# Kernel tuning notes

Hardware: AMD Instinct MI355X
Metric: run time of the kernel (lower is better)

Reference implementation:

```python
import jax, jax.numpy as jnp
import numpy as np

N_NODES = 100000
N_EDGES = 1600000


def _sage_conv(x, src, dst, W_l, W_r, b):
    """PyG SAGEConv (mean aggr): lin_l(mean of neighbor feats) + b + lin_r(x)."""
    n = x.shape[0]
    msgs = x[src]                                            # [E, F] gather
    agg = jax.ops.segment_sum(msgs, dst, num_segments=n)     # [N, F]
    cnt = jax.ops.segment_sum(jnp.ones((src.shape[0],), x.dtype), dst,
                              num_segments=n)                # [N]
    mean = agg / jnp.maximum(cnt, 1.0)[:, None]
    return mean @ W_l + b + x @ W_r


def setup_inputs() -> dict:
    key = jax.random.key(0)
    ks = jax.random.split(key, 8)
    x = jax.random.normal(ks[0], (N_NODES, 64), dtype=jnp.float32)
    edge_index = jax.random.randint(ks[1], (2, N_EDGES), 0, N_NODES, dtype=jnp.int64)
    # Glorot-ish small init for weights
    W1_l = jax.random.normal(ks[2], (64, 128), dtype=jnp.float32) * 0.1
    W1_r = jax.random.normal(ks[3], (64, 128), dtype=jnp.float32) * 0.1
    b1 = jax.random.normal(ks[4], (128,), dtype=jnp.float32) * 0.1
    W2_l = jax.random.normal(ks[5], (128, 64), dtype=jnp.float32) * 0.1
    W2_r = jax.random.normal(ks[6], (128, 64), dtype=jnp.float32) * 0.1
    b2 = jax.random.normal(ks[7], (64,), dtype=jnp.float32) * 0.1
    return {"x": x, "edge_index": edge_index, "W1_l": W1_l, "W1_r": W1_r,
            "b1": b1, "W2_l": W2_l, "W2_r": W2_r, "b2": b2}


def reference(x, edge_index, W1_l, W1_r, b1, W2_l, W2_r, b2):
    src, dst = edge_index[0], edge_index[1]
    h = jax.nn.relu(_sage_conv(x, src, dst, W1_l, W1_r, b1))  # [N, 128]
    out = _sage_conv(h, src, dst, W2_l, W2_r, b2)             # [N, 64]
    return out
```

## Files before the change

kernel.cpp:

```cpp
#include <hip/hip_runtime.h>
#include <hip/hip_bf16.h>
#include <stdint.h>


typedef unsigned short u16;
typedef __attribute__((ext_vector_type(8))) short short8;
typedef __attribute__((ext_vector_type(4))) float f32x4;

#define BSHIFT 9
#define BSIZE  512
#define CHUNK  8192
#define NCP    256

__device__ __forceinline__ float bf2f(u16 v) { return __uint_as_float(((uint32_t)v) << 16); }
__device__ __forceinline__ float bfu_lo(uint32_t u) { return __uint_as_float(u << 16); }
__device__ __forceinline__ float bfu_hi(uint32_t u) { return __uint_as_float(u & 0xffff0000u); }
__device__ __forceinline__ u16 f2bf(float f) {
    uint32_t u = __float_as_uint(f);
    return (u16)((u + 0x7fffu + ((u >> 16) & 1u)) >> 16);
}

__global__ __launch_bounds__(512) void setup_k(
    const void* __restrict__ x, const void* __restrict__ ei,
    const void* __restrict__ W1l, const void* __restrict__ W1r,
    const void* __restrict__ b1, const void* __restrict__ W2l,
    const void* __restrict__ W2r, const void* __restrict__ b2,
    u16* __restrict__ wpk, u16* __restrict__ xb,
    int* __restrict__ hist2d, int* __restrict__ flags,
    int nn, int ne, int nb, int nchunk, int ncvt,
    int c0, int c1, int c2, int c3, int c4, int c5, int c6) {
    __shared__ int sh[512];
    __shared__ int sflag;
    int bid = blockIdx.x, tid = threadIdx.x;
    if (bid < nchunk) {
        sh[tid] = 0;
        int samp = 0;
        if (tid < 32) {
            long long n32 = 2LL * ne;
            long long stride = n32 / 32; if (stride < 1) stride = 1;
            long long i = (long long)tid * stride; i |= 1;
            if (i >= n32) i = 1;
            samp = (((const int*)ei)[i] != 0);
        }
        unsigned long long m = __ballot(samp);
        if (tid == 0) sflag = (m == 0ULL) ? 1 : 0;
        __syncthreads();
        int e64 = sflag;
        int base = bid * CHUNK;
#pragma unroll
        for (int j = 0; j < 16; j++) {
            int e = base + j * 512 + tid;
            if (e < ne) {
                int dst = e64 ? (int)((const long long*)ei)[(size_t)ne + e]
                              : ((const int*)ei)[(size_t)ne + e];
                if ((unsigned)dst < (unsigned)nn) atomicAdd(&sh[dst >> BSHIFT], 1);
            }
        }
        __syncthreads();
        for (int b = tid; b < nb; b += 512)
            hist2d[b * NCP + bid] = sh[b];
    } else if (bid < nchunk + ncvt) {
        int samp = 0;
        if (tid < 32) {
            int C = c0; int stride = C / 32; if (stride < 1) stride = 1;
            long long i = (long long)tid * stride;
            if (i > C - 1) i = C - 1; i &= ~1LL;
            u16 v = ((const u16*)x)[i];
            int e = (v >> 7) & 0xFF;
            samp = ((e >= 0x50 && e <= 0x97) || v == 0) ? 1 : 0;
        }
        unsigned long long m = __ballot(samp);
        if (tid == 0) sflag = (__popcll(m) >= 24) ? 1 : 0;
        __syncthreads();
        if (sflag) return;
        int i = (bid - nchunk) * 512 + tid;
        if (i < nn * 16) {
            float4 f = ((const float4*)x)[i];
            *(ushort4*)&xb[(size_t)i * 4] =
                make_ushort4(f2bf(f.x), f2bf(f.y), f2bf(f.z), f2bf(f.w));
        }
    } else if (bid < nchunk + ncvt + 4) {
        int b = bid - nchunk - ncvt;
        const void* src = (b == 0) ? W1l : (b == 1) ? W1r : (b == 2) ? W2l : W2r;
        int C = (b == 0) ? c1 : (b == 1) ? c2 : (b == 2) ? c4 : c5;
        int samp = 0;
        if (tid < 32) {
            int stride = C / 32; if (stride < 1) stride = 1;
            long long i = (long long)tid * stride;
            if (i > C - 1) i = C - 1; i &= ~1LL;
            u16 v = ((const u16*)src)[i];
            int e = (v >> 7) & 0xFF;
            samp = ((e >= 0x50 && e <= 0x97) || v == 0) ? 1 : 0;
        }
        unsigned long long m = __ballot(samp);
        if (tid == 0) sflag = (__popcll(m) >= 24) ? 1 : 0;
        __syncthreads();
        int isbf = sflag;
        u16* dst = wpk + ((b >= 2) ? (16384 + (b - 2) * 8192) : 0);
        for (int i = tid; i < 2048; i += 512) {
            u16 v0, v1, v2, v3;
            if (isbf) {
                ushort4 u = ((const ushort4*)src)[i];
                v0 = u.x; v1 = u.y; v2 = u.z; v3 = u.w;
            } else {
                float4 u = ((const float4*)src)[i];
                v0 = f2bf(u.x); v1 = f2bf(u.y); v2 = f2bf(u.z); v3 = f2bf(u.w);
            }
            int k, n, k8;
            if (b <= 1) { k = i >> 5; n = (i & 31) * 4; k8 = (b == 1 ? 8 : 0) + (k >> 3); }
            else        { k = i >> 4; n = (i & 15) * 4; k8 = k >> 3; }
            int kc = k8 >> 2, q = k8 & 3, w = k & 7;
            int basei = ((n >> 4) * 4 + kc) * 512 + (q * 16 + (n & 15)) * 8 + w;
            dst[basei] = v0; dst[basei + 8] = v1; dst[basei + 16] = v2; dst[basei + 24] = v3;
        }
    } else {
        int a = tid >> 5, lane = tid & 31;
        if (tid < 8) sh[tid] = 0;
        __syncthreads();
        if (a < 7) {
            const void* ptrs[7] = {x, W1l, W1r, b1, W2l, W2r, b2};
            int cs[7] = {c0, c1, c2, c3, c4, c5, c6};
            int C = cs[a];
            int stride = C / 32; if (stride < 1) stride = 1;
            long long i = (long long)lane * stride;
            if (i > C - 1) i = C - 1;
            i &= ~1LL;
            u16 v = ((const u16*)ptrs[a])[i];
            int e = (v >> 7) & 0xFF;
            int sane = ((e >= 0x50 && e <= 0x97) || v == 0) ? 1 : 0;
            atomicAdd(&sh[a], sane);
        } else if (a == 7) {
            long long n32 = 2LL * ne;
            long long stride = n32 / 32; if (stride < 1) stride = 1;
            long long i = (long long)lane * stride; i |= 1;
            if (i >= n32) i = 1;
            int wv = ((const int*)ei)[i];
            atomicAdd(&sh[7], wv != 0 ? 1 : 0);
        }
        __syncthreads();
        if (tid < 7) flags[tid] = (sh[tid] >= 24) ? 1 : 0;
        if (tid == 7) flags[7] = (sh[7] == 0) ? 1 : 0;
    }
}

__global__ __launch_bounds__(256) void scan2d(
    const int* __restrict__ hist2d, int* __restrict__ base2d,
    int* __restrict__ btot, int nchunk) {
    __shared__ int t0[256];
    int b = blockIdx.x, tid = threadIdx.x;
    int v = (tid < nchunk) ? hist2d[b * NCP + tid] : 0;
    t0[tid] = v;
    __syncthreads();
    for (int d = 1; d < 256; d <<= 1) {
        int t = (tid >= d) ? t0[tid - d] : 0;
        __syncthreads();
        t0[tid] += t;
        __syncthreads();
    }
    if (tid < nchunk) base2d[b * NCP + tid] = t0[tid] - v;
    if (tid == 255) btot[b] = t0[255];
}

__global__ __launch_bounds__(512) void partition_k(
    const void* __restrict__ ei, const int* __restrict__ btot,
    const int* __restrict__ base2d,
    unsigned* __restrict__ ep, int nn, int ne, int nb) {
    __shared__ unsigned stage[CHUNK];
    __shared__ u16 ab[CHUNK];
    __shared__ int hist[512], incl[512], exl[512], gbase[512], lcur[512];
    __shared__ int e64s;
    int tid = threadIdx.x;
    int base = blockIdx.x * CHUNK;
    hist[tid] = 0;
    int samp = 0;
    if (tid < 32) {
        long long n32 = 2LL * ne;
        long long stride = n32 / 32; if (stride < 1) stride = 1;
        long long i = (long long)tid * stride; i |= 1;
        if (i >= n32) i = 1;
        samp = (((const int*)ei)[i] != 0);
    }
    unsigned long long bm = __ballot(samp);
    if (tid == 0) e64s = (bm == 0ULL) ? 1 : 0;
    __syncthreads();
    int e64 = e64s;
    unsigned pk[16]; int bk[16];
#pragma unroll
    for (int j = 0; j < 16; j++) {
        int e = base + j * 512 + tid;
        bk[j] = -1;
        pk[j] = 0;
        if (e < ne) {
            int src, dst;
            if (e64) {
                src = (int)((const long long*)ei)[e];
                dst = (int)((const long long*)ei)[(size_t)ne + e];
            } else {
                src = ((const int*)ei)[e];
                dst = ((const int*)ei)[(size_t)ne + e];
            }
            if ((unsigned)dst < (unsigned)nn) {
                if ((unsigned)src >= (unsigned)nn) src = 0;
                bk[j] = dst >> BSHIFT;
                pk[j] = (unsigned)src | ((unsigned)(dst & (BSIZE - 1)) << 17);
                atomicAdd(&hist[bk[j]], 1);
            }
        }
    }
    __syncthreads();
    incl[tid] = hist[tid];
    __syncthreads();
    for (int d = 1; d < 512; d <<= 1) {
        int t = (tid >= d) ? incl[tid - d] : 0;
        __syncthreads();
        incl[tid] += t;
        __syncthreads();
    }
    int ex = incl[tid] - hist[tid];
    exl[tid] = ex;
    lcur[tid] = ex;
    int tot = incl[511];
    __syncthreads();
    incl[tid] = (tid < nb) ? btot[tid] : 0;
    __syncthreads();
    for (int d = 1; d < 512; d <<= 1) {
        int t = (tid >= d) ? incl[tid - d] : 0;
        __syncthreads();
        incl[tid] += t;
        __syncthreads();
    }
    int bo_t = incl[tid] - ((tid < nb) ? btot[tid] : 0);
    gbase[tid] = (tid < nb) ? (bo_t + base2d[tid * NCP + blockIdx.x]) : 0;
    __syncthreads();
#pragma unroll
    for (int j = 0; j < 16; j++) {
        if (bk[j] >= 0) {
            int r = atomicAdd(&lcur[bk[j]], 1);
            stage[r] = pk[j];
            ab[r] = (u16)bk[j];
        }
    }
    __syncthreads();
    for (int j = tid; j < tot; j += 512) {
        int b = ab[j];
        ep[gbase[b] + (j - exl[b])] = stage[j];
    }
}

__global__ __launch_bounds__(512) void csr_fill2(
    const unsigned* __restrict__ ep, const int* __restrict__ btot,
    int* __restrict__ off, int* __restrict__ cnt, int* __restrict__ esrc,
    int nn, int nb) {
    __shared__ int hist[BSIZE], incl[BSIZE], lcur[BSIZE];
    int b = blockIdx.x;
    int tid = threadIdx.x;
    incl[tid] = (tid < nb) ? btot[tid] : 0;
    __syncthreads();
    for (int d = 1; d < 512; d <<= 1) {
        int t = (tid >= d) ? incl[tid - d] : 0;
        __syncthreads();
        incl[tid] += t;
        __syncthreads();
    }
    int end = incl[b];
    int beg = end - btot[b];
    __syncthreads();
    hist[tid] = 0;
    __syncthreads();
    for (int j = beg + tid; j < end; j += 512)
        atomicAdd(&hist[(ep[j] >> 17) & (BSIZE - 1)], 1);
    __syncthreads();
    incl[tid] = hist[tid];
    __syncthreads();
    for (int d = 1; d < 512; d <<= 1) {
        int t = (tid >= d) ? incl[tid - d] : 0;
        __syncthreads();
        incl[tid] += t;
        __syncthreads();
    }
    int ex = beg + incl[tid] - hist[tid];
    lcur[tid] = ex;
    int node = b * BSIZE + tid;
    if (node < nn) { off[node] = ex; cnt[node] = hist[tid]; }
    __syncthreads();
    for (int j = beg + tid; j < end; j += 512) {
        unsigned p = ep[j];
        int r = atomicAdd(&lcur[(p >> 17) & (BSIZE - 1)], 1);
        esrc[r] = (int)(p & 0x1FFFFu);
    }
}

__global__ __launch_bounds__(512, 8) void layer1(
    const void* __restrict__ x, const u16* __restrict__ xb,
    const int* __restrict__ esrc,
    const int* __restrict__ off, const int* __restrict__ cnt,
    const u16* __restrict__ w1g, const u16* __restrict__ w2lg,
    const u16* __restrict__ w2rg, const void* __restrict__ b1,
    u16* __restrict__ g, u16* __restrict__ rr,
    const int* __restrict__ flags, int nn) {
    __shared__ __align__(16) u16 wA[8 * 512];
    __shared__ float b_s[128];
    int tid = threadIdx.x;
    int node0 = blockIdx.x * 32;

    if (tid < 128) b_s[tid] = flags[3] ? bf2f(((const u16*)b1)[tid]) : ((const float*)b1)[tid];

    int grp = tid >> 4, gl = tid & 15;
    int n = node0 + grp;
    int mtile = grp >> 4, l15m = grp & 15;
    int idx_mean = (mtile * 4 + (gl >> 3)) * 512 + (((gl >> 1) & 3) * 16 + l15m) * 8 + (gl & 1) * 4;
    int idx_x = (mtile * 4 + 2 + (gl >> 3)) * 512 + (((gl >> 1) & 3) * 16 + l15m) * 8 + (gl & 1) * 4;
    const u16* xs = flags[0] ? (const u16*)x : xb;
    if (n < nn) {
        int beg = off[n], deg = cnt[n];
        float a0 = 0.f, a1 = 0.f, a2 = 0.f, a3 = 0.f;
        int i = 0;
        const u16* xbp = xs + gl * 4;
        for (; i + 16 <= deg; i += 16) {
            ushort4 v[16];
#pragma unroll
            for (int j = 0; j < 16; j++) {
                int s0 = esrc[beg + i + j];
                v[j] = *(const ushort4*)(xbp + (size_t)s0 * 64);
            }
#pragma unroll
            for (int j = 0; j < 16; j++) {
                a0 += bf2f(v[j].x); a1 += bf2f(v[j].y);
                a2 += bf2f(v[j].z); a3 += bf2f(v[j].w);
            }
        }
        for (; i + 8 <= deg; i += 8) {
            ushort4 v[8];
#pragma unroll
            for (int j = 0; j < 8; j++) {
                int s0 = esrc[beg + i + j];
                v[j] = *(const ushort4*)(xbp + (size_t)s0 * 64);
            }
#pragma unroll
            for (int j = 0; j < 8; j++) {
                a0 += bf2f(v[j].x); a1 += bf2f(v[j].y);
                a2 += bf2f(v[j].z); a3 += bf2f(v[j].w);
            }
        }
        for (; i < deg; i++) {
            int s0 = esrc[beg + i];
            ushort4 v = *(const ushort4*)(xbp + (size_t)s0 * 64);
            a0 += bf2f(v.x); a1 += bf2f(v.y); a2 += bf2f(v.z); a3 += bf2f(v.w);
        }
        float inv = 1.0f / (float)(deg > 0 ? deg : 1);
        *(ushort4*)&wA[idx_mean] =
            make_ushort4(f2bf(a0 * inv), f2bf(a1 * inv), f2bf(a2 * inv), f2bf(a3 * inv));
        *(ushort4*)&wA[idx_x] = *(const ushort4*)(xs + (size_t)n * 64 + gl * 4);
    } else {
        *(ushort4*)&wA[idx_mean] = make_ushort4(0, 0, 0, 0);
        *(ushort4*)&wA[idx_x] = make_ushort4(0, 0, 0, 0);
    }
    __syncthreads();

    int wv = tid >> 6, lane = tid & 63;
    int l15 = lane & 15, q = lane >> 4;
    f32x4 acc0 = {0.f, 0.f, 0.f, 0.f};
    f32x4 acc1 = {0.f, 0.f, 0.f, 0.f};
#pragma unroll
    for (int kc = 0; kc < 4; kc++) {
        short8 a0 = *(const short8*)&wA[(kc) * 512 + lane * 8];
        short8 a1 = *(const short8*)&wA[(4 + kc) * 512 + lane * 8];
        short8 b  = *(const short8*)&w1g[(wv * 4 + kc) * 512 + lane * 8];
        acc0 = __builtin_amdgcn_mfma_f32_16x16x32_bf16(a0, b, acc0, 0, 0, 0);
        acc1 = __builtin_amdgcn_mfma_f32_16x16x32_bf16(a1, b, acc1, 0, 0, 0);
    }
    int nc = wv * 16 + l15;
    float bias = b_s[nc];
    u16 hv0[4], hv1[4];
#pragma unroll
    for (int r = 0; r < 4; r++) {
        hv0[r] = f2bf(fmaxf(acc0[r] + bias, 0.0f));
        hv1[r] = f2bf(fmaxf(acc1[r] + bias, 0.0f));
    }
    __syncthreads();
    int kcg = wv >> 1;
    int qg  = ((wv & 1) << 1) | (l15 >> 3);
    int wg  = l15 & 7;
#pragma unroll
    for (int r = 0; r < 4; r++) {
        int m = q * 4 + r;
        wA[kcg * 512 + (qg * 16 + m) * 8 + wg]       = hv0[r];
        wA[(4 + kcg) * 512 + (qg * 16 + m) * 8 + wg] = hv1[r];
    }
    __syncthreads();
    int mt2 = wv >> 2, nt2 = wv & 3;
    f32x4 ag = {0.f, 0.f, 0.f, 0.f};
    f32x4 ar = {0.f, 0.f, 0.f, 0.f};
#pragma unroll
    for (int kc = 0; kc < 4; kc++) {
        short8 a = *(const short8*)&wA[(mt2 * 4 + kc) * 512 + lane * 8];
        short8 bl = *(const short8*)&w2lg[(nt2 * 4 + kc) * 512 + lane * 8];
        short8 br = *(const short8*)&w2rg[(nt2 * 4 + kc) * 512 + lane * 8];
        ag = __builtin_amdgcn_mfma_f32_16x16x32_bf16(a, bl, ag, 0, 0, 0);
        ar = __builtin_amdgcn_mfma_f32_16x16x32_bf16(a, br, ar, 0, 0, 0);
    }
    __syncthreads();
    int nc2 = nt2 * 16 + l15;
#pragma unroll
    for (int r = 0; r < 4; r++) {
        int m = mt2 * 16 + q * 4 + r;
        wA[m * 64 + nc2]        = f2bf(ag[r]);
        wA[2048 + m * 64 + nc2] = f2bf(ar[r]);
    }
    __syncthreads();
    int half = tid >> 8, idx = tid & 255;
    int row = idx >> 3, seg = idx & 7;
    int nd = node0 + row;
    if (nd < nn) {
        uint4 v = *(const uint4*)&wA[half * 2048 + row * 64 + seg * 8];
        u16* dst = (half ? rr : g) + (size_t)nd * 64 + seg * 8;
        *(uint4*)dst = v;
    }
}

__global__ __launch_bounds__(512, 8) void layer2(
    const u16* __restrict__ g, const u16* __restrict__ rr,
    const int* __restrict__ esrc,
    const int* __restrict__ off, const int* __restrict__ cnt,
    const void* __restrict__ b2, void* __restrict__ out,
    const int* __restrict__ flags, int nn) {
    __shared__ float b_s[64];
    int tid = threadIdx.x;
    int node0 = blockIdx.x * 32;
    int obf = flags[0];
    if (tid < 64) b_s[tid] = flags[6] ? bf2f(((const u16*)b2)[tid]) : ((const float*)b2)[tid];
    __syncthreads();

    int grp = tid >> 4, gl = tid & 15;
    int n = node0 + grp;
    if (n >= nn) return;
    int beg = off[n], deg = cnt[n];
    float a0 = 0.f, a1 = 0.f, a2 = 0.f, a3 = 0.f;
    const u16* gb = g + gl * 4;
    int i = 0;
    for (; i + 16 <= deg; i += 16) {
        uint2 v[16];
#pragma unroll
        for (int j = 0; j < 16; j++) {
            int s0 = esrc[beg + i + j];
            v[j] = *(const uint2*)(gb + (size_t)s0 * 64);
        }
#pragma unroll
        for (int j = 0; j < 16; j++) {
            a0 += bfu_lo(v[j].x); a1 += bfu_hi(v[j].x);
            a2 += bfu_lo(v[j].y); a3 += bfu_hi(v[j].y);
        }
    }
    for (; i + 8 <= deg; i += 8) {
        uint2 v[8];
#pragma unroll
        for (int j = 0; j < 8; j++) {
            int s0 = esrc[beg + i + j];
            v[j] = *(const uint2*)(gb + (size_t)s0 * 64);
        }
#pragma unroll
        for (int j = 0; j < 8; j++) {
            a0 += bfu_lo(v[j].x); a1 += bfu_hi(v[j].x);
            a2 += bfu_lo(v[j].y); a3 += bfu_hi(v[j].y);
        }
    }
    for (; i < deg; i++) {
        int s0 = esrc[beg + i];
        uint2 v = *(const uint2*)(gb + (size_t)s0 * 64);
        a0 += bfu_lo(v.x); a1 += bfu_hi(v.x);
        a2 += bfu_lo(v.y); a3 += bfu_hi(v.y);
    }
    float inv = 1.0f / (float)(deg > 0 ? deg : 1);
    uint2 rv = *(const uint2*)(rr + (size_t)n * 64 + gl * 4);
    float o0 = a0 * inv + bfu_lo(rv.x) + b_s[gl * 4 + 0];
    float o1 = a1 * inv + bfu_hi(rv.x) + b_s[gl * 4 + 1];
    float o2 = a2 * inv + bfu_lo(rv.y) + b_s[gl * 4 + 2];
    float o3 = a3 * inv + bfu_hi(rv.y) + b_s[gl * 4 + 3];
    if (obf) {
        u16* op = (u16*)out + (size_t)n * 64 + gl * 4;
        *(ushort4*)op = make_ushort4(f2bf(o0), f2bf(o1), f2bf(o2), f2bf(o3));
    } else {
        float* op = (float*)out + (size_t)n * 64 + gl * 4;
        *(float4*)op = make_float4(o0, o1, o2, o3);
    }
}

__global__ __launch_bounds__(256) void zero_out_k(u16* __restrict__ out, int n) {
    int i = blockIdx.x * 256 + threadIdx.x;
    if (i < n) out[i] = 0;
}

extern "C" void kernel_launch(void* const* d_in, const int* in_sizes, int n_in,
                              void* d_out, int out_size, void* d_ws, size_t ws_size,
                              hipStream_t stream) {
    const void* x   = d_in[0];
    const void* ei  = d_in[1];
    const void* W1l = d_in[2];
    const void* W1r = d_in[3];
    const void* b1  = d_in[4];
    const void* W2l = d_in[5];
    const void* W2r = d_in[6];
    const void* b2  = d_in[7];

    int nn = in_sizes[0] / 64;
    int ne = in_sizes[1] / 2;
    int nb = (nn + BSIZE - 1) / BSIZE;
    int nchunk = (ne + CHUNK - 1) / CHUNK;

    auto al = [](size_t v) { return (v + 255) & ~(size_t)255; };
    size_t o_flags = 0;
    size_t o_btot  = 256;
    size_t o_wpk   = al(o_btot + 512 * 4);
    size_t o_cnt   = al(o_wpk + 65536);
    size_t o_off   = al(o_cnt + (size_t)nn * 4);
    size_t o_esrc  = al(o_off + (size_t)nn * 4);
    size_t o_r     = al(o_esrc + (size_t)ne * 4);
    size_t o_xb    = al(o_r + (size_t)nn * 64 * 2);
    size_t o_g     = al(o_xb + (size_t)nn * 64 * 2);
    size_t ws_req  = o_g + (size_t)nn * 64 * 2;

    size_t o_ep   = o_r;
    size_t o_h2d  = al(o_ep + (size_t)ne * 4);
    size_t o_b2d  = al(o_h2d + (size_t)512 * NCP * 4);
    size_t ov_end = o_b2d + (size_t)512 * NCP * 4;

    bool ok = ws_size >= ws_req && nb >= 1 && nb <= 512 && nn <= 131072 &&
              nchunk <= NCP && ov_end <= o_xb;
    if (!ok) {
        zero_out_k<<<(out_size + 255) / 256, 256, 0, stream>>>((u16*)d_out, out_size);
        return;
    }

    char* ws = (char*)d_ws;
    int* flags  = (int*)(ws + o_flags);
    int* btot   = (int*)(ws + o_btot);
    u16* wpk    = (u16*)(ws + o_wpk);
    int* cnt    = (int*)(ws + o_cnt);
    int* off    = (int*)(ws + o_off);
    int* esrc   = (int*)(ws + o_esrc);
    u16* rbuf   = (u16*)(ws + o_r);
    u16* xb     = (u16*)(ws + o_xb);
    u16* gbuf   = (u16*)(ws + o_g);
    unsigned* ep = (unsigned*)(ws + o_ep);
    int* hist2d = (int*)(ws + o_h2d);
    int* base2d = (int*)(ws + o_b2d);

    int ncvt = (nn * 16 + 511) / 512;
    setup_k<<<nchunk + ncvt + 5, 512, 0, stream>>>(
        x, ei, W1l, W1r, b1, W2l, W2r, b2, wpk, xb, hist2d, flags,
        nn, ne, nb, nchunk, ncvt,
        in_sizes[0], in_sizes[2], in_sizes[3], in_sizes[4],
        in_sizes[5], in_sizes[6], in_sizes[7]);
    scan2d<<<nb, 256, 0, stream>>>(hist2d, base2d, btot, nchunk);
    partition_k<<<nchunk, 512, 0, stream>>>(ei, btot, base2d, ep, nn, ne, nb);
    csr_fill2<<<nb, 512, 0, stream>>>(ep, btot, off, cnt, esrc, nn, nb);
    int lb = (nn + 31) / 32;
    layer1<<<lb, 512, 0, stream>>>(x, xb, esrc, off, cnt,
                                   wpk, wpk + 16384, wpk + 24576, b1,
                                   gbuf, rbuf, flags, nn);
    layer2<<<lb, 512, 0, stream>>>(gbuf, rbuf, esrc, off, cnt, b2, d_out, flags, nn);
}
```

Measured before the change: 222.9 us.

## Replace two-level bucket partition CSR build with global atomic counting sort

Builds the CSR graph with per-node global atomic counts, a two-pass block scan plus fixup, and a fill pass that scatters each source into its slot through an atomic cursor. This replaces the older scheme: per-chunk bucket histograms, a 2D scan, a bucket partition and a per-bucket local sort. The aim is to remove the intermediate packed-edge buffer and the several heavy shared-memory scan kernels. In exchange it issues 1.6M global atomics twice and writes esrc in scattered order. Edge order within each node is now nondeterministic, which can change floating-point summation order and hurt gather locality.

```diff
diff --git a/kernel.cpp b/kernel.cpp
--- a/kernel.cpp
+++ b/kernel.cpp
@@ -7,10 +7,7 @@
 typedef __attribute__((ext_vector_type(8))) short short8;
 typedef __attribute__((ext_vector_type(4))) float f32x4;
 
-#define BSHIFT 9
-#define BSIZE  512
 #define CHUNK  8192
-#define NCP    256
 
 __device__ __forceinline__ float bf2f(u16 v) { return __uint_as_float(((uint32_t)v) << 16); }
 __device__ __forceinline__ float bfu_lo(uint32_t u) { return __uint_as_float(u << 16); }
@@ -20,20 +17,24 @@
     return (u16)((u + 0x7fffu + ((u >> 16) & 1u)) >> 16);
 }
 
+__global__ __launch_bounds__(256) void zero_k(int* __restrict__ cnt, int n) {
+    int i = blockIdx.x * 256 + threadIdx.x;
+    if (i < n) cnt[i] = 0;
+}
+
 __global__ __launch_bounds__(512) void setup_k(
     const void* __restrict__ x, const void* __restrict__ ei,
     const void* __restrict__ W1l, const void* __restrict__ W1r,
     const void* __restrict__ b1, const void* __restrict__ W2l,
     const void* __restrict__ W2r, const void* __restrict__ b2,
     u16* __restrict__ wpk, u16* __restrict__ xb,
-    int* __restrict__ hist2d, int* __restrict__ flags,
-    int nn, int ne, int nb, int nchunk, int ncvt,
+    int* __restrict__ cnt, int* __restrict__ flags,
+    int nn, int ne, int nchunk, int ncvt,
     int c0, int c1, int c2, int c3, int c4, int c5, int c6) {
-    __shared__ int sh[512];
+    __shared__ int sh[8];
     __shared__ int sflag;
     int bid = blockIdx.x, tid = threadIdx.x;
     if (bid < nchunk) {
-        sh[tid] = 0;
         int samp = 0;
         if (tid < 32) {
             long long n32 = 2LL * ne;
@@ -53,12 +54,9 @@
             if (e < ne) {
                 int dst = e64 ? (int)((const long long*)ei)[(size_t)ne + e]
                               : ((const int*)ei)[(size_t)ne + e];
-                if ((unsigned)dst < (unsigned)nn) atomicAdd(&sh[dst >> BSHIFT], 1);
-            }
-        }
-        __syncthreads();
-        for (int b = tid; b < nb; b += 512)
-            hist2d[b * NCP + bid] = sh[b];
+                if ((unsigned)dst < (unsigned)nn) atomicAdd(&cnt[dst], 1);
+            }
+        }
     } else if (bid < nchunk + ncvt) {
         int samp = 0;
         if (tid < 32) {
@@ -143,35 +141,53 @@
     }
 }
 
-__global__ __launch_bounds__(256) void scan2d(
-    const int* __restrict__ hist2d, int* __restrict__ base2d,
-    int* __restrict__ btot, int nchunk) {
-    __shared__ int t0[256];
+__global__ __launch_bounds__(512) void scan_nodes(
+    const int* __restrict__ cnt, int* __restrict__ off,
+    int* __restrict__ bsum, int nn) {
+    __shared__ int t0[512];
     int b = blockIdx.x, tid = threadIdx.x;
-    int v = (tid < nchunk) ? hist2d[b * NCP + tid] : 0;
+    int node = b * 512 + tid;
+    int v = (node < nn) ? cnt[node] : 0;
     t0[tid] = v;
     __syncthreads();
-    for (int d = 1; d < 256; d <<= 1) {
+    for (int d = 1; d < 512; d <<= 1) {
         int t = (tid >= d) ? t0[tid - d] : 0;
         __syncthreads();
         t0[tid] += t;
         __syncthreads();
     }
-    if (tid < nchunk) base2d[b * NCP + tid] = t0[tid] - v;
-    if (tid == 255) btot[b] = t0[255];
-}
-
-__global__ __launch_bounds__(512) void partition_k(
-    const void* __restrict__ ei, const int* __restrict__ btot,
-    const int* __restrict__ base2d,
-    unsigned* __restrict__ ep, int nn, int ne, int nb) {
-    __shared__ unsigned stage[CHUNK];
-    __shared__ u16 ab[CHUNK];
-    __shared__ int hist[512], incl[512], exl[512], gbase[512], lcur[512];
-    __shared__ int e64s;
+    if (node < nn) off[node] = t0[tid] - v;
+    if (tid == 511) bsum[b] = t0[511];
+}
+
+__global__ __launch_bounds__(512) void fixup_k(
+    int* __restrict__ off, int* __restrict__ cur,
+    const int* __restrict__ bsum, int nn, int nb) {
+    __shared__ int t0[512];
+    int b = blockIdx.x, tid = threadIdx.x;
+    int v = (tid < nb) ? bsum[tid] : 0;
+    t0[tid] = v;
+    __syncthreads();
+    for (int d = 1; d < 512; d <<= 1) {
+        int t = (tid >= d) ? t0[tid - d] : 0;
+        __syncthreads();
+        t0[tid] += t;
+        __syncthreads();
+    }
+    int base = t0[b] - bsum[b];
+    int node = b * 512 + tid;
+    if (node < nn) {
+        int o = off[node] + base;
+        off[node] = o;
+        cur[node] = o;
+    }
+}
+
+__global__ __launch_bounds__(512) void fill_k(
+    const void* __restrict__ ei, int* __restrict__ cur,
+    int* __restrict__ esrc, int nn, int ne) {
+    __shared__ int sflag;
     int tid = threadIdx.x;
-    int base = blockIdx.x * CHUNK;
-    hist[tid] = 0;
     int samp = 0;
     if (tid < 32) {
         long long n32 = 2LL * ne;
@@ -180,16 +196,14 @@
         if (i >= n32) i = 1;
         samp = (((const int*)ei)[i] != 0);
     }
-    unsigned long long bm = __ballot(samp);
-    if (tid == 0) e64s = (bm == 0ULL) ? 1 : 0;
-    __syncthreads();
-    int e64 = e64s;
-    unsigned pk[16]; int bk[16];
+    unsigned long long m = __ballot(samp);
+    if (tid == 0) sflag = (m == 0ULL) ? 1 : 0;
+    __syncthreads();
+    int e64 = sflag;
+    int base = blockIdx.x * CHUNK;
 #pragma unroll
     for (int j = 0; j < 16; j++) {
         int e = base + j * 512 + tid;
-        bk[j] = -1;
-        pk[j] = 0;
         if (e < ne) {
             int src, dst;
             if (e64) {
@@ -201,92 +215,10 @@
             }
             if ((unsigned)dst < (unsigned)nn) {
                 if ((unsigned)src >= (unsigned)nn) src = 0;
-                bk[j] = dst >> BSHIFT;
-                pk[j] = (unsigned)src | ((unsigned)(dst & (BSIZE - 1)) << 17);
-                atomicAdd(&hist[bk[j]], 1);
-            }
-        }
-    }
-    __syncthreads();
-    incl[tid] = hist[tid];
-    __syncthreads();
-    for (int d = 1; d < 512; d <<= 1) {
-        int t = (tid >= d) ? incl[tid - d] : 0;
-        __syncthreads();
-        incl[tid] += t;
-        __syncthreads();
-    }
-    int ex = incl[tid] - hist[tid];
-    exl[tid] = ex;
-    lcur[tid] = ex;
-    int tot = incl[511];
-    __syncthreads();
-    incl[tid] = (tid < nb) ? btot[tid] : 0;
-    __syncthreads();
-    for (int d = 1; d < 512; d <<= 1) {
-        int t = (tid >= d) ? incl[tid - d] : 0;
-        __syncthreads();
-        incl[tid] += t;
-        __syncthreads();
-    }
-    int bo_t = incl[tid] - ((tid < nb) ? btot[tid] : 0);
-    gbase[tid] = (tid < nb) ? (bo_t + base2d[tid * NCP + blockIdx.x]) : 0;
-    __syncthreads();
-#pragma unroll
-    for (int j = 0; j < 16; j++) {
-        if (bk[j] >= 0) {
-            int r = atomicAdd(&lcur[bk[j]], 1);
-            stage[r] = pk[j];
-            ab[r] = (u16)bk[j];
-        }
-    }
-    __syncthreads();
-    for (int j = tid; j < tot; j += 512) {
-        int b = ab[j];
-        ep[gbase[b] + (j - exl[b])] = stage[j];
-    }
-}
-
-__global__ __launch_bounds__(512) void csr_fill2(
-    const unsigned* __restrict__ ep, const int* __restrict__ btot,
-    int* __restrict__ off, int* __restrict__ cnt, int* __restrict__ esrc,
-    int nn, int nb) {
-    __shared__ int hist[BSIZE], incl[BSIZE], lcur[BSIZE];
-    int b = blockIdx.x;
-    int tid = threadIdx.x;
-    incl[tid] = (tid < nb) ? btot[tid] : 0;
-    __syncthreads();
-    for (int d = 1; d < 512; d <<= 1) {
-        int t = (tid >= d) ? incl[tid - d] : 0;
-        __syncthreads();
-        incl[tid] += t;
-        __syncthreads();
-    }
-    int end = incl[b];
-    int beg = end - btot[b];
-    __syncthreads();
-    hist[tid] = 0;
-    __syncthreads();
-    for (int j = beg + tid; j < end; j += 512)
-        atomicAdd(&hist[(ep[j] >> 17) & (BSIZE - 1)], 1);
-    __syncthreads();
-    incl[tid] = hist[tid];
-    __syncthreads();
-    for (int d = 1; d < 512; d <<= 1) {
-        int t = (tid >= d) ? incl[tid - d] : 0;
-        __syncthreads();
-        incl[tid] += t;
-        __syncthreads();
-    }
-    int ex = beg + incl[tid] - hist[tid];
-    lcur[tid] = ex;
-    int node = b * BSIZE + tid;
-    if (node < nn) { off[node] = ex; cnt[node] = hist[tid]; }
-    __syncthreads();
-    for (int j = beg + tid; j < end; j += 512) {
-        unsigned p = ep[j];
-        int r = atomicAdd(&lcur[(p >> 17) & (BSIZE - 1)], 1);
-        esrc[r] = (int)(p & 0x1FFFFu);
+                int r = atomicAdd(&cur[dst], 1);
+                esrc[r] = src;
+            }
+        }
     }
 }
 
@@ -504,28 +436,23 @@
 
     int nn = in_sizes[0] / 64;
     int ne = in_sizes[1] / 2;
-    int nb = (nn + BSIZE - 1) / BSIZE;
     int nchunk = (ne + CHUNK - 1) / CHUNK;
+    int nb2 = (nn + 511) / 512;
 
     auto al = [](size_t v) { return (v + 255) & ~(size_t)255; };
     size_t o_flags = 0;
-    size_t o_btot  = 256;
-    size_t o_wpk   = al(o_btot + 512 * 4);
+    size_t o_bsum  = 256;
+    size_t o_wpk   = al(o_bsum + 512 * 4);
     size_t o_cnt   = al(o_wpk + 65536);
     size_t o_off   = al(o_cnt + (size_t)nn * 4);
-    size_t o_esrc  = al(o_off + (size_t)nn * 4);
+    size_t o_cur   = al(o_off + (size_t)nn * 4);
+    size_t o_esrc  = al(o_cur + (size_t)nn * 4);
     size_t o_r     = al(o_esrc + (size_t)ne * 4);
     size_t o_xb    = al(o_r + (size_t)nn * 64 * 2);
     size_t o_g     = al(o_xb + (size_t)nn * 64 * 2);
     size_t ws_req  = o_g + (size_t)nn * 64 * 2;
 
-    size_t o_ep   = o_r;
-    size_t o_h2d  = al(o_ep + (size_t)ne * 4);
-    size_t o_b2d  = al(o_h2d + (size_t)512 * NCP * 4);
-    size_t ov_end = o_b2d + (size_t)512 * NCP * 4;
-
-    bool ok = ws_size >= ws_req && nb >= 1 && nb <= 512 && nn <= 131072 &&
-              nchunk <= NCP && ov_end <= o_xb;
+    bool ok = ws_size >= ws_req && nb2 >= 1 && nb2 <= 512 && nn <= 131072;
     if (!ok) {
         zero_out_k<<<(out_size + 255) / 256, 256, 0, stream>>>((u16*)d_out, out_size);
         return;
@@ -533,27 +460,26 @@
 
     char* ws = (char*)d_ws;
     int* flags  = (int*)(ws + o_flags);
-    int* btot   = (int*)(ws + o_btot);
+    int* bsum   = (int*)(ws + o_bsum);
     u16* wpk    = (u16*)(ws + o_wpk);
     int* cnt    = (int*)(ws + o_cnt);
     int* off    = (int*)(ws + o_off);
+    int* cur    = (int*)(ws + o_cur);
     int* esrc   = (int*)(ws + o_esrc);
     u16* rbuf   = (u16*)(ws + o_r);
     u16* xb     = (u16*)(ws + o_xb);
     u16* gbuf   = (u16*)(ws + o_g);
-    unsigned* ep = (unsigned*)(ws + o_ep);
-    int* hist2d = (int*)(ws + o_h2d);
-    int* base2d = (int*)(ws + o_b2d);
 
     int ncvt = (nn * 16 + 511) / 512;
+    zero_k<<<(nn + 255) / 256, 256, 0, stream>>>(cnt, nn);
     setup_k<<<nchunk + ncvt + 5, 512, 0, stream>>>(
-        x, ei, W1l, W1r, b1, W2l, W2r, b2, wpk, xb, hist2d, flags,
-        nn, ne, nb, nchunk, ncvt,
+        x, ei, W1l, W1r, b1, W2l, W2r, b2, wpk, xb, cnt, flags,
+        nn, ne, nchunk, ncvt,
         in_sizes[0], in_sizes[2], in_sizes[3], in_sizes[4],
         in_sizes[5], in_sizes[6], in_sizes[7]);
-    scan2d<<<nb, 256, 0, stream>>>(hist2d, base2d, btot, nchunk);
-    partition_k<<<nchunk, 512, 0, stream>>>(ei, btot, base2d, ep, nn, ne, nb);
-    csr_fill2<<<nb, 512, 0, stream>>>(ep, btot, off, cnt, esrc, nn, nb);
+    scan_nodes<<<nb2, 512, 0, stream>>>(cnt, off, bsum, nn);
+    fixup_k<<<nb2, 512, 0, stream>>>(off, cur, bsum, nn, nb2);
+    fill_k<<<nchunk, 512, 0, stream>>>(ei, cur, esrc, nn, ne);
     int lb = (nn + 31) / 32;
     layer1<<<lb, 512, 0, stream>>>(x, xb, esrc, off, cnt,
                                    wpk, wpk + 16384, wpk + 24576, b1,
```

After: 323.7 us. +45.2%, slower.
